# Performance work log

Hardware: AMD Instinct MI355X
Metric: run time of the kernel (lower is better)

Reference implementation:

```python
import jax, jax.numpy as jnp
import numpy as np

T, B, V, E, HID, K = 1024, 128, 65536, 128, 256, 64
H = HID // 2  # per-direction LSTM hidden


def setup_inputs() -> dict:
    key = jax.random.key(0)
    ks = jax.random.split(key, 18)
    s = 0.05
    f32 = jnp.float32
    return {
        "kmers": jax.random.randint(ks[0], (T, B), 0, V),
        "tags": jax.random.randint(ks[1], (B,), 0, K),
        "emb": jax.random.normal(ks[2], (V, E), f32) * s,
        "w_ih_f": jax.random.normal(ks[3], (4 * H, E), f32) * s,
        "w_hh_f": jax.random.normal(ks[4], (4 * H, H), f32) * s,
        "b_ih_f": jax.random.normal(ks[5], (4 * H,), f32) * s,
        "b_hh_f": jax.random.normal(ks[6], (4 * H,), f32) * s,
        "w_ih_b": jax.random.normal(ks[7], (4 * H, E), f32) * s,
        "w_hh_b": jax.random.normal(ks[8], (4 * H, H), f32) * s,
        "b_ih_b": jax.random.normal(ks[9], (4 * H,), f32) * s,
        "b_hh_b": jax.random.normal(ks[10], (4 * H,), f32) * s,
        "w_proj": jax.random.normal(ks[11], (K, HID), f32) * s,
        "b_proj": jax.random.normal(ks[12], (K,), f32) * s,
        "start_trans": jax.random.uniform(ks[13], (K,), f32, -0.1, 0.1),
        "end_trans": jax.random.uniform(ks[14], (K,), f32, -0.1, 0.1),
        "trans": jax.random.uniform(ks[15], (K, K), f32, -0.1, 0.1),
    }


def _lstm_dir(x, w_ih, w_hh, b_ih, b_hh):
    # x: [T, B, E] -> hidden states [T, B, H]; PyTorch gate order i,f,g,o
    b = b_ih + b_hh
    xg = jnp.einsum('tbe,ge->tbg', x, w_ih) + b  # precompute input gates
    Bd = x.shape[1]
    Hd = w_hh.shape[1]
    def step(carry, g_in):
        h, c = carry
        g = g_in + h @ w_hh.T
        i, f, gg, o = jnp.split(g, 4, axis=-1)
        c = jax.nn.sigmoid(f) * c + jax.nn.sigmoid(i) * jnp.tanh(gg)
        h = jax.nn.sigmoid(o) * jnp.tanh(c)
        return (h, c), h
    init = (jnp.zeros((Bd, Hd), x.dtype), jnp.zeros((Bd, Hd), x.dtype))
    _, hs = jax.lax.scan(step, init, xg)
    return hs


def reference(kmers, tags, emb, w_ih_f, w_hh_f, b_ih_f, b_hh_f,
              w_ih_b, w_hh_b, b_ih_b, b_hh_b, w_proj, b_proj,
              start_trans, end_trans, trans):
    x = emb[kmers]  # [T, B, E]
    h_f = _lstm_dir(x, w_ih_f, w_hh_f, b_ih_f, b_hh_f)
    h_b = _lstm_dir(x[::-1], w_ih_b, w_hh_b, b_ih_b, b_hh_b)[::-1]
    out = jnp.concatenate([h_f, h_b], axis=-1)  # [T, B, HID]
    emissions = jnp.einsum('tbh,kh->tbk', out, w_proj) + b_proj  # [T, B, K]

    # tags repeated along time (original: tags.repeat(sent_size, 1))
    tags_seq = jnp.broadcast_to(tags[None, :], (emissions.shape[0], tags.shape[0]))

    # CRF numerator: score of given tag sequence (full mask)
    em_sel = jnp.take_along_axis(emissions, tags_seq[:, :, None], axis=2)[..., 0]  # [T, B]
    numerator = (start_trans[tags_seq[0]] + em_sel.sum(0)
                 + trans[tags_seq[:-1], tags_seq[1:]].sum(0)
                 + end_trans[tags_seq[-1]])  # [B]

    # CRF denominator: forward algorithm (log partition)
    def fwd_step(score, em_t):
        # score: [B, K] -> logsumexp over previous tag
        nxt = jax.nn.logsumexp(score[:, :, None] + trans[None, :, :] + em_t[:, None, :], axis=1)
        return nxt, None
    init = start_trans[None, :] + emissions[0]  # [B, K]
    final, _ = jax.lax.scan(fwd_step, init, emissions[1:])
    denominator = jax.nn.logsumexp(final + end_trans[None, :], axis=1)  # [B]

    # torchcrf default reduction='sum'; module returns negated llh
    return (denominator - numerator).sum()
```

## Files before the change

kernel.cpp:

```cpp
#include <hip/hip_runtime.h>
#include <hip/hip_bf16.h>

typedef _Float16 half8_t __attribute__((ext_vector_type(8)));
typedef _Float16 half4_t __attribute__((ext_vector_type(4)));
typedef _Float16 half2_t __attribute__((ext_vector_type(2)));
typedef float float4_t __attribute__((ext_vector_type(4)));
typedef unsigned int uint2_t __attribute__((ext_vector_type(2)));

#define TT 1024
#define BB 128
#define EE 128
#define HH 128
#define NTAG 64
#define ASTR 144

__device__ __forceinline__ float fast_exp(float x) {
  return __builtin_amdgcn_exp2f(x * 1.44269504088896f);
}
__device__ __forceinline__ void lds_barrier() {
  asm volatile("s_waitcnt lgkmcnt(0)\n\ts_barrier" ::: "memory");
}
__device__ __forceinline__ half2_t cvt_pk(float a, float b) {
  return __builtin_bit_cast(half2_t, __builtin_amdgcn_cvt_pkrtz(a, b));
}
__device__ __forceinline__ half2_t h2bc(float v) {
  _Float16 h = (_Float16)v;
  half2_t r; r[0] = h; r[1] = h;
  return r;
}
__device__ __forceinline__ float quad_max4(float v) {
  unsigned a = __builtin_bit_cast(unsigned, v);
  uint2_t r = __builtin_amdgcn_permlane32_swap(a, a, false, false);
  float m = fmaxf(__builtin_bit_cast(float, r[0]), __builtin_bit_cast(float, r[1]));
  unsigned b = __builtin_bit_cast(unsigned, m);
  uint2_t s = __builtin_amdgcn_permlane16_swap(b, b, false, false);
  return fmaxf(__builtin_bit_cast(float, s[0]), __builtin_bit_cast(float, s[1]));
}
__device__ __forceinline__ half2_t tanh6(half2_t x) {
  half2_t y = __builtin_elementwise_min(__builtin_elementwise_max(x, h2bc(-1.6f)), h2bc(1.6f));
  half2_t u = y * y;
  half2_t p = u * h2bc(0.04667f) + h2bc(-0.28507f);
  p = u * p + h2bc(1.0f);
  return y * p;
}
__device__ __forceinline__ half2_t sig6(half2_t x) {
  half2_t y = __builtin_elementwise_min(__builtin_elementwise_max(x, h2bc(-3.2f)), h2bc(3.2f));
  half2_t u = y * y;
  half2_t q = u * h2bc(0.00072921875f) + h2bc(-0.017816875f);
  q = u * q + h2bc(0.25f);
  return y * q + h2bc(0.5f);
}

__global__ __launch_bounds__(256) void init_kernel(float4_t* __restrict__ p) {
  p[blockIdx.x * 256 + threadIdx.x] = (float4_t){0.f, 0.f, 0.f, 0.f};
}

__global__ __launch_bounds__(256) void embed_kernel(const int* __restrict__ kmers,
                                                    const float* __restrict__ emb,
                                                    half4_t* __restrict__ x) {
  const int g = blockIdx.x * 256 + threadIdx.x;
  const int row = g >> 5, seg = g & 31;
  const int km = kmers[row];
  const float4_t v = ((const float4_t*)(emb + (size_t)km * EE))[seg];
  half4_t o;
  o[0] = (_Float16)v[0]; o[1] = (_Float16)v[1];
  o[2] = (_Float16)v[2]; o[3] = (_Float16)v[3];
  x[(size_t)row * 32 + seg] = o;
}

__device__ __forceinline__ void xg_body(
    int wg, const _Float16* __restrict__ x,
    const float* __restrict__ w_ih_f, const float* __restrict__ b_ih_f, const float* __restrict__ b_hh_f,
    const float* __restrict__ w_ih_b, const float* __restrict__ b_ih_b, const float* __restrict__ b_hh_b,
    _Float16* __restrict__ xgbuf, int s, int Tseg) {
  const int nt = Tseg >> 4;
  const int dir = wg / (8 * nt);
  const int rem = wg - dir * 8 * nt;
  const int chunk = rem / nt;
  const int tb = rem - chunk * nt;
  const int tid = threadIdx.x;
  const int wave = tid >> 6, lane = tid & 63;
  const int n16 = lane & 15, quad = lane >> 4;

  const float* wih = dir ? w_ih_b : w_ih_f;
  const float* bih = dir ? b_ih_b : b_ih_f;
  const float* bhh = dir ? b_hh_b : b_hh_f;

  half8_t wf[4][4];
#pragma unroll
  for (int g = 0; g < 4; ++g) {
    const int row = g * HH + wave * 16 + n16;
#pragma unroll
    for (int kf = 0; kf < 4; ++kf) {
      const float* src = wih + row * EE + kf * 32 + quad * 8;
#pragma unroll
      for (int i = 0; i < 8; ++i) wf[g][kf][i] = (_Float16)src[i];
    }
  }
  float4_t bias4[4];
#pragma unroll
  for (int g = 0; g < 4; ++g) {
    const int row = g * HH + wave * 16 + quad * 4;
    const float4_t bi = *(const float4_t*)(bih + row);
    const float4_t bh = *(const float4_t*)(bhh + row);
    bias4[g] = bi + bh;
  }

  const int l0 = tb * 16;
  half8_t xb[4];
  {
    const int te = dir ? (TT - 1 - (s * Tseg + l0)) : (s * Tseg + l0);
#pragma unroll
    for (int kf = 0; kf < 4; ++kf)
      xb[kf] = *(const half8_t*)(x + ((size_t)te * BB + chunk * 16 + n16) * EE + kf * 32 + quad * 8);
  }
  for (int u = 0; u < 16; ++u) {
    const int l = l0 + u;
    half8_t xn[4] = {};
    if (u < 15) {
      const int tn = dir ? (TT - 1 - (s * Tseg + l + 1)) : (s * Tseg + l + 1);
#pragma unroll
      for (int kf = 0; kf < 4; ++kf)
        xn[kf] = *(const half8_t*)(x + ((size_t)tn * BB + chunk * 16 + n16) * EE + kf * 32 + quad * 8);
    }
    float4_t acc[4];
#pragma unroll
    for (int g = 0; g < 4; ++g) acc[g] = bias4[g];
#pragma unroll
    for (int kf = 0; kf < 4; ++kf)
#pragma unroll
      for (int g = 0; g < 4; ++g)
        acc[g] = __builtin_amdgcn_mfma_f32_16x16x32_f16(wf[g][kf], xb[kf], acc[g], 0, 0, 0);
    half8_t ho0, ho1;
#pragma unroll
    for (int r = 0; r < 4; ++r) {
      ho0[r] = (_Float16)acc[0][r];
      ho0[4 + r] = (_Float16)acc[1][r];
      ho1[r] = (_Float16)acc[2][r];
      ho1[4 + r] = (_Float16)acc[3][r];
    }
    _Float16* ob = xgbuf + (size_t)dir * Tseg * 65536 + (size_t)l * 65536 + chunk * 8192 +
                   wave * 1024 + lane * 16;
    *(half8_t*)ob = ho0;
    *(half8_t*)(ob + 8) = ho1;
#pragma unroll
    for (int kf = 0; kf < 4; ++kf) xb[kf] = xn[kf];
  }
}

__global__ __launch_bounds__(512) void xg_kernel(
    const _Float16* __restrict__ x,
    const float* __restrict__ w_ih_f, const float* __restrict__ b_ih_f, const float* __restrict__ b_hh_f,
    const float* __restrict__ w_ih_b, const float* __restrict__ b_ih_b, const float* __restrict__ b_hh_b,
    _Float16* __restrict__ xgbuf, int s, int Tseg) {
  xg_body(blockIdx.x, x, w_ih_f, b_ih_f, b_hh_f, w_ih_b, b_ih_b, b_hh_b, xgbuf, s, Tseg);
}

__global__ __launch_bounds__(512, 2) void lstm_xg_kernel(
    const _Float16* __restrict__ xgrd, _Float16* __restrict__ xgwr,
    const _Float16* __restrict__ x,
    const float* __restrict__ w_hh_f, const float* __restrict__ w_hh_b,
    const float* __restrict__ w_ih_f, const float* __restrict__ b_ih_f, const float* __restrict__ b_hh_f,
    const float* __restrict__ w_ih_b, const float* __restrict__ b_ih_b, const float* __restrict__ b_hh_b,
    _Float16* __restrict__ h_cat, _Float16* __restrict__ h_state, float* __restrict__ c_state,
    int s, int sx, int Tseg) {
  __shared__ _Float16 A[2][16 * ASTR];
  if (blockIdx.x >= 16) {
    xg_body(blockIdx.x - 16, x, w_ih_f, b_ih_f, b_hh_f, w_ih_b, b_ih_b, b_hh_b, xgwr, sx, Tseg);
    return;
  }
  const int wg = blockIdx.x;
  const int dir = wg >> 3, chunk = wg & 7;
  const int b0 = chunk * 16;
  const float* w_hh = dir ? w_hh_b : w_hh_f;
  const int tid = threadIdx.x;
  const int wave = tid >> 6, lane = tid & 63;
  const int n16 = lane & 15, quad = lane >> 4;

  half8_t wf[4][4];
#pragma unroll
  for (int g = 0; g < 4; ++g) {
    const int row = g * HH + wave * 16 + n16;
#pragma unroll
    for (int kf = 0; kf < 4; ++kf) {
      const float* src = w_hh + row * HH + kf * 32 + quad * 8;
#pragma unroll
      for (int i = 0; i < 8; ++i) wf[g][kf][i] = (_Float16)src[i];
    }
  }
  const int sidx = ((wg * 8 + wave) * 64 + lane) * 4;
  half4_t h4 = *(const half4_t*)(h_state + sidx);
  float4_t c4 = *(const float4_t*)(c_state + sidx);
  half2_t c2[2];
  c2[0] = cvt_pk(c4[0], c4[1]);
  c2[1] = cvt_pk(c4[2], c4[3]);
  *(half4_t*)(&A[0][n16 * ASTR + wave * 16 + quad * 4]) = h4;

  const _Float16* xgw =
      xgrd + (size_t)dir * Tseg * 65536 + chunk * 8192 + wave * 1024 + (size_t)lane * 16;
  half4_t hlast = h4;
  const float4_t z4 = {0.f, 0.f, 0.f, 0.f};
  const int te0 = dir ? (TT - 1 - s * Tseg) : (s * Tseg);
  _Float16* gp_run =
      h_cat + ((size_t)te0 * BB + b0 + n16) * 256 + dir * HH + wave * 16 + quad * 4;
  const ptrdiff_t dstep = dir ? -(ptrdiff_t)32768 : (ptrdiff_t)32768;

  half8_t pf0[4], pf1[4];
#pragma unroll
  for (int j = 0; j < 4; ++j) {
    const _Float16* p = xgw + (size_t)j * 65536;
    pf0[j] = *(const half8_t*)p;
    pf1[j] = *(const half8_t*)(p + 8);
  }

#define LSTM_STEP(AB, AN, X0, X1)                                                          \
  {                                                                                        \
    const _Float16* Abp = &AB[0];                                                          \
    _Float16* Anp = &AN[0];                                                                \
    half8_t hb0 = *(const half8_t*)(Abp + n16 * ASTR + 0 * 32 + quad * 8);                 \
    half8_t hb1 = *(const half8_t*)(Abp + n16 * ASTR + 1 * 32 + quad * 8);                 \
    half8_t hb2 = *(const half8_t*)(Abp + n16 * ASTR + 2 * 32 + quad * 8);                 \
    half8_t hb3 = *(const half8_t*)(Abp + n16 * ASTR + 3 * 32 + quad * 8);                 \
    float4_t acc[4];                                                                       \
    _Pragma("unroll") for (int g = 0; g < 4; ++g) {                                        \
      acc[g] = __builtin_amdgcn_mfma_f32_16x16x32_f16(wf[g][0], hb0, z4, 0, 0, 0);         \
    }                                                                                      \
    _Pragma("unroll") for (int g = 0; g < 4; ++g) {                                        \
      acc[g] = __builtin_amdgcn_mfma_f32_16x16x32_f16(wf[g][1], hb1, acc[g], 0, 0, 0);     \
    }                                                                                      \
    _Pragma("unroll") for (int g = 0; g < 4; ++g) {                                        \
      acc[g] = __builtin_amdgcn_mfma_f32_16x16x32_f16(wf[g][2], hb2, acc[g], 0, 0, 0);     \
    }                                                                                      \
    _Pragma("unroll") for (int g = 0; g < 4; ++g) {                                        \
      acc[g] = __builtin_amdgcn_mfma_f32_16x16x32_f16(wf[g][3], hb3, acc[g], 0, 0, 0);     \
    }                                                                                      \
    const half2_t* x0p = (const half2_t*)&X0;                                              \
    const half2_t* x1p = (const half2_t*)&X1;                                              \
    half4_t hstore;                                                                        \
    _Pragma("unroll") for (int p = 0; p < 2; ++p) {                                        \
      const half2_t i_ = sig6(cvt_pk(acc[0][2 * p], acc[0][2 * p + 1]) + x0p[p]);          \
      const half2_t f_ = sig6(cvt_pk(acc[1][2 * p], acc[1][2 * p + 1]) + x0p[2 + p]);      \
      const half2_t g_ = tanh6(cvt_pk(acc[2][2 * p], acc[2][2 * p + 1]) + x1p[p]);         \
      const half2_t o_ = sig6(cvt_pk(acc[3][2 * p], acc[3][2 * p + 1]) + x1p[2 + p]);      \
      c2[p] = f_ * c2[p] + i_ * g_;                                                        \
      const half2_t hh = o_ * tanh6(c2[p]);                                                \
      hstore[2 * p] = hh[0];                                                               \
      hstore[2 * p + 1] = hh[1];                                                           \
    }                                                                                      \
    *(half4_t*)(Anp + n16 * ASTR + wave * 16 + quad * 4) = hstore;                         \
    *(half4_t*)gp_run = hstore;                                                            \
    hlast = hstore;                                                                        \
  }

  for (int il = 0; il < Tseg - 4; il += 4) {
#pragma unroll
    for (int j = 0; j < 4; ++j) {
      lds_barrier();
      if (j & 1) {
        LSTM_STEP(A[1], A[0], pf0[j], pf1[j]);
      } else {
        LSTM_STEP(A[0], A[1], pf0[j], pf1[j]);
      }
      const _Float16* p = xgw + (size_t)(il + j + 4) * 65536;
      pf0[j] = *(const half8_t*)p;
      pf1[j] = *(const half8_t*)(p + 8);
      gp_run += dstep;
    }
  }
#pragma unroll
  for (int j = 0; j < 4; ++j) {
    lds_barrier();
    if (j & 1) {
      LSTM_STEP(A[1], A[0], pf0[j], pf1[j]);
    } else {
      LSTM_STEP(A[0], A[1], pf0[j], pf1[j]);
    }
    gp_run += dstep;
  }
#undef LSTM_STEP

  *(half4_t*)(h_state + sidx) = hlast;
  c4[0] = (float)c2[0][0]; c4[1] = (float)c2[0][1];
  c4[2] = (float)c2[1][0]; c4[3] = (float)c2[1][1];
  *(float4_t*)(c_state + sidx) = c4;
}

__global__ __launch_bounds__(256) void emis_kernel(const _Float16* __restrict__ h_cat,
                                                   const float* __restrict__ w_proj,
                                                   const float* __restrict__ b_proj,
                                                   float* __restrict__ em,
                                                   _Float16* __restrict__ expem) {
  const int tid = threadIdx.x;
  const int wave = tid >> 6, lane = tid & 63;
  const int n16 = lane & 15, quad = lane >> 4;
  const size_t row0 = (size_t)blockIdx.x * 64 + wave * 16;

  half8_t bf[4][8];
#pragma unroll
  for (int nt = 0; nt < 4; ++nt) {
    const float* wp = w_proj + (nt * 16 + n16) * 256;
#pragma unroll
    for (int kf = 0; kf < 8; ++kf) {
      const int kb = kf * 32 + quad * 8;
#pragma unroll
      for (int i = 0; i < 8; ++i) bf[nt][kf][i] = (_Float16)wp[kb + i];
    }
  }
  float4_t acc[4];
#pragma unroll
  for (int nt = 0; nt < 4; ++nt) {
    const float bv = b_proj[nt * 16 + n16];
    acc[nt] = (float4_t){bv, bv, bv, bv};
  }
#pragma unroll
  for (int kf = 0; kf < 8; ++kf) {
    half8_t af = *(const half8_t*)(h_cat + (row0 + n16) * 256 + kf * 32 + quad * 8);
#pragma unroll
    for (int nt = 0; nt < 4; ++nt)
      acc[nt] = __builtin_amdgcn_mfma_f32_16x16x32_f16(af, bf[nt][kf], acc[nt], 0, 0, 0);
  }
#pragma unroll
  for (int nt = 0; nt < 4; ++nt)
#pragma unroll
    for (int r = 0; r < 4; ++r) {
      const size_t idx = (row0 + quad * 4 + r) * NTAG + nt * 16 + n16;
      em[idx] = acc[nt][r];
      expem[idx] = (_Float16)fast_exp(acc[nt][r]);
    }
}

__global__ __launch_bounds__(64) void crf_kernel(const float* __restrict__ em,
                                                 const _Float16* __restrict__ expem,
                                                 const float* __restrict__ trans,
                                                 const float* __restrict__ start_trans,
                                                 const float* __restrict__ end_trans,
                                                 _Float16* __restrict__ amid,
                                                 float* __restrict__ scmid) {
  const int lane = threadIdx.x;
  const int n16 = lane & 15, quad = lane >> 4;
  const int side = blockIdx.x >> 3;
  const int bg = blockIdx.x & 7;
  const int gb = bg * 16 + n16;

  half8_t efA[4][2];
#pragma unroll
  for (int mt = 0; mt < 4; ++mt)
#pragma unroll
    for (int kf = 0; kf < 2; ++kf)
#pragma unroll
      for (int i = 0; i < 8; ++i) {
        const int m = mt * 16 + n16, k = kf * 32 + quad * 8 + i;
        const float tv = side ? trans[m * NTAG + k] : trans[k * NTAG + m];
        efA[mt][kf][i] = (_Float16)(fast_exp(tv) * 0.015625f);
      }

  float sv[16];
#pragma unroll
  for (int kf = 0; kf < 2; ++kf) {
    const int j0 = kf * 32 + quad * 8;
#pragma unroll
    for (int i = 0; i < 8; ++i)
      sv[kf * 8 + i] =
          side ? end_trans[j0 + i] : (start_trans[j0 + i] + em[(size_t)gb * NTAG + j0 + i]);
  }
  float m0;
  {
    float mx[8];
#pragma unroll
    for (int i = 0; i < 8; ++i) mx[i] = fmaxf(sv[i], sv[8 + i]);
#pragma unroll
    for (int i = 0; i < 4; ++i) mx[i] = fmaxf(mx[i], mx[4 + i]);
    m0 = fmaxf(fmaxf(mx[0], mx[1]), fmaxf(mx[2], mx[3]));
    m0 = quad_max4(m0);
  }
  half8_t pb[2];
#pragma unroll
  for (int kf = 0; kf < 2; ++kf)
#pragma unroll
    for (int i = 0; i < 8; ++i) pb[kf][i] = (_Float16)fast_exp(sv[kf * 8 + i] - m0);
  float lz2 = 0.f;
  const float4_t z4 = {0.f, 0.f, 0.f, 0.f};
  const _Float16* exb = expem + (size_t)gb * NTAG;

#define CRF_CORE(PB0, PB1)                                                                 \
    float4_t a0 = __builtin_amdgcn_mfma_f32_16x16x32_f16(efA[0][0], PB0, z4, 0, 0, 0);     \
    float4_t a1 = __builtin_amdgcn_mfma_f32_16x16x32_f16(efA[1][0], PB0, z4, 0, 0, 0);     \
    float4_t a2 = __builtin_amdgcn_mfma_f32_16x16x32_f16(efA[2][0], PB0, z4, 0, 0, 0);     \
    float4_t a3 = __builtin_amdgcn_mfma_f32_16x16x32_f16(efA[3][0], PB0, z4, 0, 0, 0);     \
    a0 = __builtin_amdgcn_mfma_f32_16x16x32_f16(efA[0][1], PB1, a0, 0, 0, 0);              \
    a1 = __builtin_amdgcn_mfma_f32_16x16x32_f16(efA[1][1], PB1, a1, 0, 0, 0);              \
    a2 = __builtin_amdgcn_mfma_f32_16x16x32_f16(efA[2][1], PB1, a2, 0, 0, 0);              \
    a3 = __builtin_amdgcn_mfma_f32_16x16x32_f16(efA[3][1], PB1, a3, 0, 0, 0);              \
    half2_t dpk[4][2];                                                                     \
    dpk[0][0] = cvt_pk(a0[0], a0[1]); dpk[0][1] = cvt_pk(a0[2], a0[3]);                    \
    dpk[1][0] = cvt_pk(a1[0], a1[1]); dpk[1][1] = cvt_pk(a1[2], a1[3]);                    \
    dpk[2][0] = cvt_pk(a2[0], a2[1]); dpk[2][1] = cvt_pk(a2[2], a2[3]);                    \
    dpk[3][0] = cvt_pk(a3[0], a3[1]); dpk[3][1] = cvt_pk(a3[2], a3[3]);                    \
    half2_t ww[2][4];                                                                      \
    _Pragma("unroll") for (int kf = 0; kf < 2; ++kf)                                       \
      _Pragma("unroll") for (int p = 0; p < 2; ++p) {                                      \
        const unsigned Xu = __builtin_bit_cast(unsigned, dpk[2 * kf][p]);                  \
        const unsigned Yu = __builtin_bit_cast(unsigned, dpk[2 * kf + 1][p]);              \
        uint2_t r1 = __builtin_amdgcn_permlane32_swap(Xu, Yu, false, false);               \
        uint2_t r2 = __builtin_amdgcn_permlane16_swap(r1[0], r1[1], false, false);         \
        ww[kf][p] = __builtin_bit_cast(half2_t, r2[0]);                                    \
        ww[kf][2 + p] = __builtin_bit_cast(half2_t, r2[1]);                                \
      }

#define CRF_RESCALE(TCUR)                                                                  \
    if (((TCUR) & 15) == 0) {                                                              \
      half2_t* pw0 = (half2_t*)&pb[0];                                                     \
      half2_t* pw1 = (half2_t*)&pb[1];                                                     \
      half2_t m2 = __builtin_elementwise_max(pw0[0], pw0[1]);                              \
      m2 = __builtin_elementwise_max(m2, __builtin_elementwise_max(pw0[2], pw0[3]));       \
      m2 = __builtin_elementwise_max(m2, __builtin_elementwise_max(pw1[0], pw1[1]));       \
      m2 = __builtin_elementwise_max(m2, __builtin_elementwise_max(pw1[2], pw1[3]));       \
      float mm = fmaxf((float)m2[0], (float)m2[1]);                                        \
      mm = quad_max4(mm);                                                                  \
      lz2 += __builtin_amdgcn_logf(mm);                                                    \
      const half2_t rc = h2bc(__builtin_amdgcn_rcpf(mm));                                  \
      _Pragma("unroll") for (int j2 = 0; j2 < 4; ++j2) { pw0[j2] *= rc; pw1[j2] *= rc; }   \
    }

#define FWD_STEP(TCUR, GC0, GC1)                                                           \
  {                                                                                        \
    CRF_CORE(pb[0], pb[1])                                                                 \
    const half2_t* gw0 = (const half2_t*)&GC0;                                             \
    const half2_t* gw1 = (const half2_t*)&GC1;                                             \
    half2_t* pw0 = (half2_t*)&pb[0];                                                       \
    half2_t* pw1 = (half2_t*)&pb[1];                                                       \
    _Pragma("unroll") for (int w2 = 0; w2 < 4; ++w2) {                                     \
      pw0[w2] = ww[0][w2] * gw0[w2];                                                       \
      pw1[w2] = ww[1][w2] * gw1[w2];                                                       \
    }                                                                                      \
    CRF_RESCALE(TCUR)                                                                      \
  }

#define BWD_STEP(TCUR, GC0, GC1)                                                           \
  {                                                                                        \
    const half8_t pg0 = pb[0] * GC0;                                                       \
    const half8_t pg1 = pb[1] * GC1;                                                       \
    CRF_CORE(pg0, pg1)                                                                     \
    half2_t* pw0 = (half2_t*)&pb[0];                                                       \
    half2_t* pw1 = (half2_t*)&pb[1];                                                       \
    _Pragma("unroll") for (int w2 = 0; w2 < 4; ++w2) {                                     \
      pw0[w2] = ww[0][w2];                                                                 \
      pw1[w2] = ww[1][w2];                                                                 \
    }                                                                                      \
    CRF_RESCALE(TCUR)                                                                      \
  }

  half8_t pre0[8], pre1[8];
  if (side == 0) {
#pragma unroll
    for (int j = 0; j < 8; ++j) {
      pre0[j] = *(const half8_t*)(exb + (size_t)(1 + j) * 8192 + quad * 8);
      pre1[j] = *(const half8_t*)(exb + (size_t)(1 + j) * 8192 + 32 + quad * 8);
    }
    int t = 1;
    for (int grp = 0; grp < 64; ++grp) {
#pragma unroll
      for (int j = 0; j < 8; ++j) {
        const half8_t gc0 = pre0[j], gc1 = pre1[j];
        int tf = t + 8; tf = tf > 1023 ? 1023 : tf;
        pre0[j] = *(const half8_t*)(exb + (size_t)tf * 8192 + quad * 8);
        pre1[j] = *(const half8_t*)(exb + (size_t)tf * 8192 + 32 + quad * 8);
        FWD_STEP(t, gc0, gc1)
        ++t;
      }
    }
  } else {
#pragma unroll
    for (int j = 0; j < 8; ++j) {
      pre0[j] = *(const half8_t*)(exb + (size_t)(1023 - j) * 8192 + quad * 8);
      pre1[j] = *(const half8_t*)(exb + (size_t)(1023 - j) * 8192 + 32 + quad * 8);
    }
    int t = 1023;
    for (int grp = 0; grp < 63; ++grp) {
#pragma unroll
      for (int j = 0; j < 8; ++j) {
        const half8_t gc0 = pre0[j], gc1 = pre1[j];
        int tf = t - 8; tf = tf < 0 ? 0 : tf;
        pre0[j] = *(const half8_t*)(exb + (size_t)tf * 8192 + quad * 8);
        pre1[j] = *(const half8_t*)(exb + (size_t)tf * 8192 + 32 + quad * 8);
        BWD_STEP(t, gc0, gc1)
        --t;
      }
    }
    for (; t >= 513; --t) {
      const half8_t gc0 = *(const half8_t*)(exb + (size_t)t * 8192 + quad * 8);
      const half8_t gc1 = *(const half8_t*)(exb + (size_t)t * 8192 + 32 + quad * 8);
      BWD_STEP(t, gc0, gc1)
    }
  }
#undef FWD_STEP
#undef BWD_STEP
#undef CRF_RESCALE
#undef CRF_CORE

  _Float16* ap = amid + (size_t)(side * BB + gb) * NTAG;
  *(half8_t*)(ap + quad * 8) = pb[0];
  *(half8_t*)(ap + 32 + quad * 8) = pb[1];
  if (quad == 0)
    scmid[side * BB + gb] = m0 + 0.693147180559945f * lz2;
}

__global__ __launch_bounds__(256) void numer_kernel(const float* __restrict__ em,
                                                    const int* __restrict__ tags,
                                                    const float* __restrict__ trans,
                                                    const float* __restrict__ start_trans,
                                                    const float* __restrict__ end_trans,
                                                    float* __restrict__ num) {
  const int b = blockIdx.x;
  const int tg = tags[b];
  float acc = 0.f;
  for (int t = threadIdx.x; t < TT; t += 256)
    acc += em[((size_t)t * BB + b) * NTAG + tg];
#pragma unroll
  for (int off = 32; off > 0; off >>= 1) acc += __shfl_xor(acc, off, 64);
  __shared__ float red[4];
  if ((threadIdx.x & 63) == 0) red[threadIdx.x >> 6] = acc;
  __syncthreads();
  if (threadIdx.x == 0) {
    const float tot = red[0] + red[1] + red[2] + red[3];
    num[b] = start_trans[tg] + end_trans[tg] + 1023.0f * trans[tg * NTAG + tg] + tot;
  }
}

__global__ __launch_bounds__(128) void final_kernel(const _Float16* __restrict__ amid,
                                                    const float* __restrict__ scmid,
                                                    const float* __restrict__ num,
                                                    float* __restrict__ out) {
  const int b = threadIdx.x;
  const _Float16* af = amid + (size_t)b * NTAG;
  const _Float16* bf = amid + (size_t)(BB + b) * NTAG;
  float dot = 0.f;
#pragma unroll
  for (int kf = 0; kf < 8; ++kf) {
    const half8_t av = *(const half8_t*)(af + kf * 8);
    const half8_t bv = *(const half8_t*)(bf + kf * 8);
#pragma unroll
    for (int i = 0; i < 8; ++i) dot += (float)av[i] * (float)bv[i];
  }
  const float denomv = scmid[b] + scmid[BB + b] +
                       0.693147180559945f * (6138.0f + __builtin_amdgcn_logf(dot));
  float v = denomv - num[b];
#pragma unroll
  for (int off = 32; off > 0; off >>= 1) v += __shfl_xor(v, off, 64);
  __shared__ float red[2];
  if ((b & 63) == 0) red[b >> 6] = v;
  __syncthreads();
  if (b == 0) out[0] = red[0] + red[1];
}

extern "C" void kernel_launch(void* const* d_in, const int* in_sizes, int n_in,
                              void* d_out, int out_size, void* d_ws, size_t ws_size,
                              hipStream_t stream) {
  const int* kmers = (const int*)d_in[0];
  const int* tags = (const int*)d_in[1];
  const float* emb = (const float*)d_in[2];
  const float* w_ih_f = (const float*)d_in[3];
  const float* w_hh_f = (const float*)d_in[4];
  const float* b_ih_f = (const float*)d_in[5];
  const float* b_hh_f = (const float*)d_in[6];
  const float* w_ih_b = (const float*)d_in[7];
  const float* w_hh_b = (const float*)d_in[8];
  const float* b_ih_b = (const float*)d_in[9];
  const float* b_hh_b = (const float*)d_in[10];
  const float* w_proj = (const float*)d_in[11];
  const float* b_proj = (const float*)d_in[12];
  const float* start_trans = (const float*)d_in[13];
  const float* end_trans = (const float*)d_in[14];
  const float* trans = (const float*)d_in[15];

  char* ws = (char*)d_ws;
  half4_t* x = (half4_t*)ws;
  _Float16* h_cat = (_Float16*)(ws + 33554432);
  float* em = (float*)ws;
  float* out = (float*)d_out;

  const bool fused = ws_size >= 235078656ull;
  if (fused) {
    const int Tseg = 256;
    _Float16* buf0 = (_Float16*)(ws + 100663296);
    _Float16* buf1 = (_Float16*)(ws + 100663296 + 67108864);
    _Float16* expem = (_Float16*)(ws + 100663296);
    _Float16* h_state = (_Float16*)(ws + 100663296 + 134217728);
    float* c_state = (float*)(ws + 100663296 + 134217728 + 65536);
    _Float16* amid = (_Float16*)(ws + 100663296 + 134217728);
    float* scmid = (float*)(ws + 100663296 + 134217728 + 32768);
    float* num = (float*)(ws + 100663296 + 134217728 + 196608);

    hipLaunchKernelGGL(init_kernel, dim3(48), dim3(256), 0, stream, (float4_t*)h_state);
    hipLaunchKernelGGL(embed_kernel, dim3(16384), dim3(256), 0, stream, kmers, emb, x);
    hipLaunchKernelGGL(xg_kernel, dim3(Tseg), dim3(512), 0, stream, (const _Float16*)x,
                       w_ih_f, b_ih_f, b_hh_f, w_ih_b, b_ih_b, b_hh_b, buf0, 0, Tseg);
    for (int s = 0; s < 3; ++s) {
      _Float16* rd = (s & 1) ? buf1 : buf0;
      _Float16* wr = (s & 1) ? buf0 : buf1;
      hipLaunchKernelGGL(lstm_xg_kernel, dim3(16 + Tseg), dim3(512), 0, stream,
                         (const _Float16*)rd, wr, (const _Float16*)x, w_hh_f, w_hh_b,
                         w_ih_f, b_ih_f, b_hh_f, w_ih_b, b_ih_b, b_hh_b,
                         h_cat, h_state, c_state, s, s + 1, Tseg);
    }
    hipLaunchKernelGGL(lstm_xg_kernel, dim3(16), dim3(512), 0, stream,
                       (const _Float16*)buf1, buf0, (const _Float16*)x, w_hh_f, w_hh_b,
                       w_ih_f, b_ih_f, b_hh_f, w_ih_b, b_ih_b, b_hh_b,
                       h_cat, h_state, c_state, 3, 0, Tseg);
    hipLaunchKernelGGL(emis_kernel, dim3(2048), dim3(256), 0, stream, h_cat, w_proj, b_proj, em,
                       expem);
    hipLaunchKernelGGL(crf_kernel, dim3(16), dim3(64), 0, stream, em, (const _Float16*)expem,
                       trans, start_trans, end_trans, amid, scmid);
    hipLaunchKernelGGL(numer_kernel, dim3(128), dim3(256), 0, stream, em, tags, trans,
                       start_trans, end_trans, num);
    hipLaunchKernelGGL(final_kernel, dim3(1), dim3(128), 0, stream, amid, scmid, num, out);
  } else {
    int nseg;
    if (ws_size >= 167969792ull) nseg = 4;
    else if (ws_size >= 134415360ull) nseg = 8;
    else nseg = 16;
    const int Tseg = TT / nseg;
    const size_t xg_bytes = 268435456ull / (size_t)nseg;
    _Float16* xgbuf = (_Float16*)(ws + 100663296);
    _Float16* expem = (_Float16*)(ws + 100663296);
    _Float16* h_state = (_Float16*)(ws + 100663296 + xg_bytes);
    float* c_state = (float*)(ws + 100663296 + xg_bytes + 65536);
    _Float16* amid = (_Float16*)(ws + 100663296 + xg_bytes);
    float* scmid = (float*)(ws + 100663296 + xg_bytes + 32768);
    float* num = (float*)(ws + 100663296 + xg_bytes + 196608);

    hipLaunchKernelGGL(init_kernel, dim3(48), dim3(256), 0, stream, (float4_t*)h_state);
    hipLaunchKernelGGL(embed_kernel, dim3(16384), dim3(256), 0, stream, kmers, emb, x);
    for (int s = 0; s < nseg; ++s) {
      hipLaunchKernelGGL(xg_kernel, dim3(Tseg), dim3(512), 0, stream, (const _Float16*)x,
                         w_ih_f, b_ih_f, b_hh_f, w_ih_b, b_ih_b, b_hh_b, xgbuf, s, Tseg);
      hipLaunchKernelGGL(lstm_xg_kernel, dim3(16), dim3(512), 0, stream,
                         (const _Float16*)xgbuf, xgbuf, (const _Float16*)x, w_hh_f, w_hh_b,
                         w_ih_f, b_ih_f, b_hh_f, w_ih_b, b_ih_b, b_hh_b,
                         h_cat, h_state, c_state, s, s, Tseg);
    }
    hipLaunchKernelGGL(emis_kernel, dim3(2048), dim3(256), 0, stream, h_cat, w_proj, b_proj, em,
                       expem);
    hipLaunchKernelGGL(crf_kernel, dim3(16), dim3(64), 0, stream, em, (const _Float16*)expem,
                       trans, start_trans, end_trans, amid, scmid);
    hipLaunchKernelGGL(numer_kernel, dim3(128), dim3(256), 0, stream, em, tags, trans,
                       start_trans, end_trans, num);
    hipLaunchKernelGGL(final_kernel, dim3(1), dim3(128), 0, stream, amid, scmid, num, out);
  }
}
```

Before: 954.2 us.

## Parallelize CRF forward recursion via segmented transfer-matrix products and merge

Replaces the 16-block sequential CRF forward/backward scan with 2048 blocks, each computing the 64x64 product of scaled transition-times-emission matrices over a 64-step time segment per batch element, starting from the identity. A new merge kernel chains the 16 segment matrices per batch element with a vector, tracking log scales. The numerator computation is folded into extra blocks of the same launch. The intent is to cut the serial CRF latency tail, which used only 16 wavefronts. In exchange each block does four times the MFMA work of a vector recursion, and fp16 matrix products with periodic rescaling risk precision loss.

```diff
diff --git a/kernel.cpp b/kernel.cpp
--- a/kernel.cpp
+++ b/kernel.cpp
@@ -20,12 +20,22 @@
 __device__ __forceinline__ void lds_barrier() {
   asm volatile("s_waitcnt lgkmcnt(0)\n\ts_barrier" ::: "memory");
 }
+__device__ __forceinline__ void lds_fence() {
+  asm volatile("s_waitcnt lgkmcnt(0)" ::: "memory");
+}
 __device__ __forceinline__ half2_t cvt_pk(float a, float b) {
   return __builtin_bit_cast(half2_t, __builtin_amdgcn_cvt_pkrtz(a, b));
 }
 __device__ __forceinline__ half2_t h2bc(float v) {
   _Float16 h = (_Float16)v;
   half2_t r; r[0] = h; r[1] = h;
+  return r;
+}
+__device__ __forceinline__ half8_t h8bc(float v) {
+  _Float16 h = (_Float16)v;
+  half8_t r;
+#pragma unroll
+  for (int i = 0; i < 8; ++i) r[i] = h;
   return r;
 }
 __device__ __forceinline__ float quad_max4(float v) {
@@ -329,18 +339,31 @@
     }
 }
 
-__global__ __launch_bounds__(64) void crf_kernel(const float* __restrict__ em,
-                                                 const _Float16* __restrict__ expem,
-                                                 const float* __restrict__ trans,
-                                                 const float* __restrict__ start_trans,
-                                                 const float* __restrict__ end_trans,
-                                                 _Float16* __restrict__ amid,
-                                                 float* __restrict__ scmid) {
+__global__ __launch_bounds__(64) void mcrf_kernel(const float* __restrict__ em,
+                                                  const _Float16* __restrict__ expem,
+                                                  const float* __restrict__ trans,
+                                                  const int* __restrict__ tags,
+                                                  const float* __restrict__ start_trans,
+                                                  const float* __restrict__ end_trans,
+                                                  _Float16* __restrict__ Nbuf,
+                                                  float* __restrict__ lzbuf,
+                                                  float* __restrict__ num) {
   const int lane = threadIdx.x;
+  if (blockIdx.x >= 2048) {
+    const int nb = blockIdx.x - 2048;
+    const int tg = tags[nb];
+    float acc = 0.f;
+    for (int t = lane; t < TT; t += 64)
+      acc += em[((size_t)t * BB + nb) * NTAG + tg];
+#pragma unroll
+    for (int off = 32; off > 0; off >>= 1) acc += __shfl_xor(acc, off, 64);
+    if (lane == 0)
+      num[nb] = start_trans[tg] + end_trans[tg] + 1023.0f * trans[tg * NTAG + tg] + acc;
+    return;
+  }
   const int n16 = lane & 15, quad = lane >> 4;
-  const int side = blockIdx.x >> 3;
-  const int bg = blockIdx.x & 7;
-  const int gb = bg * 16 + n16;
+  const int b = blockIdx.x >> 4;
+  const int s = blockIdx.x & 15;
 
   half8_t efA[4][2];
 #pragma unroll
@@ -350,39 +373,28 @@
 #pragma unroll
       for (int i = 0; i < 8; ++i) {
         const int m = mt * 16 + n16, k = kf * 32 + quad * 8 + i;
-        const float tv = side ? trans[m * NTAG + k] : trans[k * NTAG + m];
-        efA[mt][kf][i] = (_Float16)(fast_exp(tv) * 0.015625f);
+        efA[mt][kf][i] = (_Float16)(fast_exp(trans[k * NTAG + m]) * 0.015625f);
       }
 
-  float sv[16];
-#pragma unroll
-  for (int kf = 0; kf < 2; ++kf) {
-    const int j0 = kf * 32 + quad * 8;
-#pragma unroll
-    for (int i = 0; i < 8; ++i)
-      sv[kf * 8 + i] =
-          side ? end_trans[j0 + i] : (start_trans[j0 + i] + em[(size_t)gb * NTAG + j0 + i]);
-  }
-  float m0;
-  {
-    float mx[8];
-#pragma unroll
-    for (int i = 0; i < 8; ++i) mx[i] = fmaxf(sv[i], sv[8 + i]);
-#pragma unroll
-    for (int i = 0; i < 4; ++i) mx[i] = fmaxf(mx[i], mx[4 + i]);
-    m0 = fmaxf(fmaxf(mx[0], mx[1]), fmaxf(mx[2], mx[3]));
-    m0 = quad_max4(m0);
-  }
-  half8_t pb[2];
-#pragma unroll
-  for (int kf = 0; kf < 2; ++kf)
-#pragma unroll
-    for (int i = 0; i < 8; ++i) pb[kf][i] = (_Float16)fast_exp(sv[kf * 8 + i] - m0);
+  half8_t pb[4][2];
+#pragma unroll
+  for (int tile = 0; tile < 4; ++tile)
+#pragma unroll
+    for (int kf = 0; kf < 2; ++kf)
+#pragma unroll
+      for (int i = 0; i < 8; ++i) {
+        const int k = kf * 32 + quad * 8 + i;
+        pb[tile][kf][i] = (_Float16)((k == tile * 16 + n16) ? 1.f : 0.f);
+      }
+
   float lz2 = 0.f;
   const float4_t z4 = {0.f, 0.f, 0.f, 0.f};
-  const _Float16* exb = expem + (size_t)gb * NTAG;
-
-#define CRF_CORE(PB0, PB1)                                                                 \
+  const _Float16* exb = expem + (size_t)b * NTAG;
+  const int t0 = s * 64 + 1;
+  const int nsteps = (s == 15) ? 63 : 64;
+
+#define MCRF_CORE(PB0, PB1, NB0, NB1)                                                      \
+  {                                                                                        \
     float4_t a0 = __builtin_amdgcn_mfma_f32_16x16x32_f16(efA[0][0], PB0, z4, 0, 0, 0);     \
     float4_t a1 = __builtin_amdgcn_mfma_f32_16x16x32_f16(efA[1][0], PB0, z4, 0, 0, 0);     \
     float4_t a2 = __builtin_amdgcn_mfma_f32_16x16x32_f16(efA[2][0], PB0, z4, 0, 0, 0);     \
@@ -396,161 +408,143 @@
     dpk[1][0] = cvt_pk(a1[0], a1[1]); dpk[1][1] = cvt_pk(a1[2], a1[3]);                    \
     dpk[2][0] = cvt_pk(a2[0], a2[1]); dpk[2][1] = cvt_pk(a2[2], a2[3]);                    \
     dpk[3][0] = cvt_pk(a3[0], a3[1]); dpk[3][1] = cvt_pk(a3[2], a3[3]);                    \
-    half2_t ww[2][4];                                                                      \
-    _Pragma("unroll") for (int kf = 0; kf < 2; ++kf)                                       \
+    half2_t* wwp0 = (half2_t*)&NB0;                                                        \
+    half2_t* wwp1 = (half2_t*)&NB1;                                                        \
+    _Pragma("unroll") for (int kf = 0; kf < 2; ++kf) {                                     \
+      half2_t* wp = kf ? wwp1 : wwp0;                                                      \
       _Pragma("unroll") for (int p = 0; p < 2; ++p) {                                      \
         const unsigned Xu = __builtin_bit_cast(unsigned, dpk[2 * kf][p]);                  \
         const unsigned Yu = __builtin_bit_cast(unsigned, dpk[2 * kf + 1][p]);              \
         uint2_t r1 = __builtin_amdgcn_permlane32_swap(Xu, Yu, false, false);               \
         uint2_t r2 = __builtin_amdgcn_permlane16_swap(r1[0], r1[1], false, false);         \
-        ww[kf][p] = __builtin_bit_cast(half2_t, r2[0]);                                    \
-        ww[kf][2 + p] = __builtin_bit_cast(half2_t, r2[1]);                                \
-      }
-
-#define CRF_RESCALE(TCUR)                                                                  \
-    if (((TCUR) & 15) == 0) {                                                              \
-      half2_t* pw0 = (half2_t*)&pb[0];                                                     \
-      half2_t* pw1 = (half2_t*)&pb[1];                                                     \
-      half2_t m2 = __builtin_elementwise_max(pw0[0], pw0[1]);                              \
-      m2 = __builtin_elementwise_max(m2, __builtin_elementwise_max(pw0[2], pw0[3]));       \
-      m2 = __builtin_elementwise_max(m2, __builtin_elementwise_max(pw1[0], pw1[1]));       \
-      m2 = __builtin_elementwise_max(m2, __builtin_elementwise_max(pw1[2], pw1[3]));       \
-      float mm = fmaxf((float)m2[0], (float)m2[1]);                                        \
+        wp[p] = __builtin_bit_cast(half2_t, r2[0]);                                        \
+        wp[2 + p] = __builtin_bit_cast(half2_t, r2[1]);                                    \
+      }                                                                                    \
+    }                                                                                      \
+  }
+
+#define MSTEP(GC0, GC1, IT)                                                                \
+  {                                                                                        \
+    _Pragma("unroll") for (int tile = 0; tile < 4; ++tile) {                               \
+      half8_t nb0, nb1;                                                                    \
+      MCRF_CORE(pb[tile][0], pb[tile][1], nb0, nb1)                                        \
+      pb[tile][0] = nb0 * GC0;                                                             \
+      pb[tile][1] = nb1 * GC1;                                                             \
+    }                                                                                      \
+    if (((IT) & 15) == 15) {                                                               \
+      half8_t m8 = __builtin_elementwise_max(pb[0][0], pb[0][1]);                          \
+      m8 = __builtin_elementwise_max(m8, __builtin_elementwise_max(pb[1][0], pb[1][1]));   \
+      m8 = __builtin_elementwise_max(m8, __builtin_elementwise_max(pb[2][0], pb[2][1]));   \
+      m8 = __builtin_elementwise_max(m8, __builtin_elementwise_max(pb[3][0], pb[3][1]));   \
+      float mm = (float)m8[0];                                                             \
+      _Pragma("unroll") for (int i = 1; i < 8; ++i) mm = fmaxf(mm, (float)m8[i]);          \
       mm = quad_max4(mm);                                                                  \
+      mm = fmaxf(mm, __shfl_xor(mm, 1, 64));                                               \
+      mm = fmaxf(mm, __shfl_xor(mm, 2, 64));                                               \
+      mm = fmaxf(mm, __shfl_xor(mm, 4, 64));                                               \
+      mm = fmaxf(mm, __shfl_xor(mm, 8, 64));                                               \
       lz2 += __builtin_amdgcn_logf(mm);                                                    \
-      const half2_t rc = h2bc(__builtin_amdgcn_rcpf(mm));                                  \
-      _Pragma("unroll") for (int j2 = 0; j2 < 4; ++j2) { pw0[j2] *= rc; pw1[j2] *= rc; }   \
-    }
-
-#define FWD_STEP(TCUR, GC0, GC1)                                                           \
-  {                                                                                        \
-    CRF_CORE(pb[0], pb[1])                                                                 \
-    const half2_t* gw0 = (const half2_t*)&GC0;                                             \
-    const half2_t* gw1 = (const half2_t*)&GC1;                                             \
-    half2_t* pw0 = (half2_t*)&pb[0];                                                       \
-    half2_t* pw1 = (half2_t*)&pb[1];                                                       \
-    _Pragma("unroll") for (int w2 = 0; w2 < 4; ++w2) {                                     \
-      pw0[w2] = ww[0][w2] * gw0[w2];                                                       \
-      pw1[w2] = ww[1][w2] * gw1[w2];                                                       \
-    }                                                                                      \
-    CRF_RESCALE(TCUR)                                                                      \
-  }
-
-#define BWD_STEP(TCUR, GC0, GC1)                                                           \
-  {                                                                                        \
-    const half8_t pg0 = pb[0] * GC0;                                                       \
-    const half8_t pg1 = pb[1] * GC1;                                                       \
-    CRF_CORE(pg0, pg1)                                                                     \
-    half2_t* pw0 = (half2_t*)&pb[0];                                                       \
-    half2_t* pw1 = (half2_t*)&pb[1];                                                       \
-    _Pragma("unroll") for (int w2 = 0; w2 < 4; ++w2) {                                     \
-      pw0[w2] = ww[0][w2];                                                                 \
-      pw1[w2] = ww[1][w2];                                                                 \
-    }                                                                                      \
-    CRF_RESCALE(TCUR)                                                                      \
-  }
-
-  half8_t pre0[8], pre1[8];
-  if (side == 0) {
-#pragma unroll
-    for (int j = 0; j < 8; ++j) {
-      pre0[j] = *(const half8_t*)(exb + (size_t)(1 + j) * 8192 + quad * 8);
-      pre1[j] = *(const half8_t*)(exb + (size_t)(1 + j) * 8192 + 32 + quad * 8);
-    }
-    int t = 1;
-    for (int grp = 0; grp < 64; ++grp) {
-#pragma unroll
-      for (int j = 0; j < 8; ++j) {
-        const half8_t gc0 = pre0[j], gc1 = pre1[j];
-        int tf = t + 8; tf = tf > 1023 ? 1023 : tf;
-        pre0[j] = *(const half8_t*)(exb + (size_t)tf * 8192 + quad * 8);
-        pre1[j] = *(const half8_t*)(exb + (size_t)tf * 8192 + 32 + quad * 8);
-        FWD_STEP(t, gc0, gc1)
-        ++t;
-      }
-    }
-  } else {
-#pragma unroll
-    for (int j = 0; j < 8; ++j) {
-      pre0[j] = *(const half8_t*)(exb + (size_t)(1023 - j) * 8192 + quad * 8);
-      pre1[j] = *(const half8_t*)(exb + (size_t)(1023 - j) * 8192 + 32 + quad * 8);
-    }
-    int t = 1023;
-    for (int grp = 0; grp < 63; ++grp) {
-#pragma unroll
-      for (int j = 0; j < 8; ++j) {
-        const half8_t gc0 = pre0[j], gc1 = pre1[j];
-        int tf = t - 8; tf = tf < 0 ? 0 : tf;
-        pre0[j] = *(const half8_t*)(exb + (size_t)tf * 8192 + quad * 8);
-        pre1[j] = *(const half8_t*)(exb + (size_t)tf * 8192 + 32 + quad * 8);
-        BWD_STEP(t, gc0, gc1)
-        --t;
-      }
-    }
-    for (; t >= 513; --t) {
-      const half8_t gc0 = *(const half8_t*)(exb + (size_t)t * 8192 + quad * 8);
-      const half8_t gc1 = *(const half8_t*)(exb + (size_t)t * 8192 + 32 + quad * 8);
-      BWD_STEP(t, gc0, gc1)
-    }
-  }
-#undef FWD_STEP
-#undef BWD_STEP
-#undef CRF_RESCALE
-#undef CRF_CORE
-
-  _Float16* ap = amid + (size_t)(side * BB + gb) * NTAG;
-  *(half8_t*)(ap + quad * 8) = pb[0];
-  *(half8_t*)(ap + 32 + quad * 8) = pb[1];
-  if (quad == 0)
-    scmid[side * BB + gb] = m0 + 0.693147180559945f * lz2;
-}
-
-__global__ __launch_bounds__(256) void numer_kernel(const float* __restrict__ em,
-                                                    const int* __restrict__ tags,
-                                                    const float* __restrict__ trans,
-                                                    const float* __restrict__ start_trans,
-                                                    const float* __restrict__ end_trans,
-                                                    float* __restrict__ num) {
-  const int b = blockIdx.x;
-  const int tg = tags[b];
-  float acc = 0.f;
-  for (int t = threadIdx.x; t < TT; t += 256)
-    acc += em[((size_t)t * BB + b) * NTAG + tg];
-#pragma unroll
-  for (int off = 32; off > 0; off >>= 1) acc += __shfl_xor(acc, off, 64);
-  __shared__ float red[4];
-  if ((threadIdx.x & 63) == 0) red[threadIdx.x >> 6] = acc;
-  __syncthreads();
-  if (threadIdx.x == 0) {
-    const float tot = red[0] + red[1] + red[2] + red[3];
-    num[b] = start_trans[tg] + end_trans[tg] + 1023.0f * trans[tg * NTAG + tg] + tot;
-  }
-}
-
-__global__ __launch_bounds__(128) void final_kernel(const _Float16* __restrict__ amid,
-                                                    const float* __restrict__ scmid,
+      const half8_t rc8 = h8bc(__builtin_amdgcn_rcpf(mm));                                 \
+      _Pragma("unroll") for (int tile = 0; tile < 4; ++tile) {                             \
+        pb[tile][0] *= rc8;                                                                \
+        pb[tile][1] *= rc8;                                                                \
+      }                                                                                    \
+    }                                                                                      \
+  }
+
+  half8_t pre0[4], pre1[4];
+#pragma unroll
+  for (int j = 0; j < 4; ++j) {
+    const size_t tt = (size_t)(t0 + j) * 8192;
+    pre0[j] = *(const half8_t*)(exb + tt + quad * 8);
+    pre1[j] = *(const half8_t*)(exb + tt + 32 + quad * 8);
+  }
+  int it = 0;
+  const int full4 = nsteps >> 2;
+  for (int grp = 0; grp < full4; ++grp) {
+#pragma unroll
+    for (int j = 0; j < 4; ++j) {
+      const half8_t gc0 = pre0[j], gc1 = pre1[j];
+      int tf = t0 + it + 4;
+      tf = tf > 1023 ? 1023 : tf;
+      const size_t tt = (size_t)tf * 8192;
+      pre0[j] = *(const half8_t*)(exb + tt + quad * 8);
+      pre1[j] = *(const half8_t*)(exb + tt + 32 + quad * 8);
+      MSTEP(gc0, gc1, it)
+      ++it;
+    }
+  }
+  for (; it < nsteps; ++it) {
+    const size_t tt = (size_t)(t0 + it) * 8192;
+    const half8_t gc0 = *(const half8_t*)(exb + tt + quad * 8);
+    const half8_t gc1 = *(const half8_t*)(exb + tt + 32 + quad * 8);
+    MSTEP(gc0, gc1, it)
+  }
+#undef MSTEP
+#undef MCRF_CORE
+
+  _Float16* nb = Nbuf + ((size_t)b * 16 + s) * 4096;
+#pragma unroll
+  for (int tile = 0; tile < 4; ++tile) {
+    const int col = tile * 16 + n16;
+#pragma unroll
+    for (int kf = 0; kf < 2; ++kf)
+      *(half8_t*)(nb + (size_t)col * 64 + kf * 32 + quad * 8) = pb[tile][kf];
+  }
+  if (lane == 0) lzbuf[b * 16 + s] = lz2;
+}
+
+__global__ __launch_bounds__(64) void merge_kernel(const _Float16* __restrict__ Nbuf,
+                                                   const float* __restrict__ lzbuf,
+                                                   const float* __restrict__ em,
+                                                   const float* __restrict__ start_trans,
+                                                   const float* __restrict__ end_trans,
+                                                   float* __restrict__ denom) {
+  const int b = blockIdx.x, m = threadIdx.x;
+  __shared__ float w[64];
+  float L2 = 0.f;
+  w[m] = fast_exp(end_trans[m]);
+  for (int s = 15; s >= 0; --s) {
+    lds_fence();
+    const _Float16* row = Nbuf + (((size_t)b * 16 + s) * 64 + m) * 64;
+    float acc = 0.f;
+#pragma unroll
+    for (int kf = 0; kf < 8; ++kf) {
+      const half8_t rv = *(const half8_t*)(row + kf * 8);
+#pragma unroll
+      for (int i = 0; i < 8; ++i) acc += (float)rv[i] * w[kf * 8 + i];
+    }
+    float mx = acc;
+#pragma unroll
+    for (int off = 32; off > 0; off >>= 1) mx = fmaxf(mx, __shfl_xor(mx, off, 64));
+    L2 += __builtin_amdgcn_logf(mx) + lzbuf[b * 16 + s];
+    const float inv = __builtin_amdgcn_rcpf(mx);
+    lds_fence();
+    w[m] = acc * inv;
+  }
+  lds_fence();
+  const float sv = start_trans[m] + em[(size_t)b * NTAG + m];
+  float m0 = sv;
+#pragma unroll
+  for (int off = 32; off > 0; off >>= 1) m0 = fmaxf(m0, __shfl_xor(m0, off, 64));
+  float z = fast_exp(sv - m0) * w[m];
+#pragma unroll
+  for (int off = 32; off > 0; off >>= 1) z += __shfl_xor(z, off, 64);
+  if (m == 0)
+    denom[b] = m0 + 0.693147180559945f * (L2 + 6138.0f + __builtin_amdgcn_logf(z));
+}
+
+__global__ __launch_bounds__(128) void final_kernel(const float* __restrict__ denom,
                                                     const float* __restrict__ num,
                                                     float* __restrict__ out) {
-  const int b = threadIdx.x;
-  const _Float16* af = amid + (size_t)b * NTAG;
-  const _Float16* bf = amid + (size_t)(BB + b) * NTAG;
-  float dot = 0.f;
-#pragma unroll
-  for (int kf = 0; kf < 8; ++kf) {
-    const half8_t av = *(const half8_t*)(af + kf * 8);
-    const half8_t bv = *(const half8_t*)(bf + kf * 8);
-#pragma unroll
-    for (int i = 0; i < 8; ++i) dot += (float)av[i] * (float)bv[i];
-  }
-  const float denomv = scmid[b] + scmid[BB + b] +
-                       0.693147180559945f * (6138.0f + __builtin_amdgcn_logf(dot));
-  float v = denomv - num[b];
+  const int tid = threadIdx.x;
+  float v = denom[tid] - num[tid];
 #pragma unroll
   for (int off = 32; off > 0; off >>= 1) v += __shfl_xor(v, off, 64);
   __shared__ float red[2];
-  if ((b & 63) == 0) red[b >> 6] = v;
+  if ((tid & 63) == 0) red[tid >> 6] = v;
   __syncthreads();
-  if (b == 0) out[0] = red[0] + red[1];
+  if (tid == 0) out[0] = red[0] + red[1];
 }
 
 extern "C" void kernel_launch(void* const* d_in, const int* in_sizes, int n_in,
@@ -578,6 +572,10 @@
   _Float16* h_cat = (_Float16*)(ws + 33554432);
   float* em = (float*)ws;
   float* out = (float*)d_out;
+  _Float16* Nbuf = (_Float16*)(ws + 33554432);
+  float* lzbuf = (float*)(ws + 33554432 + 16777216);
+  float* denom = (float*)(ws + 33554432 + 16785408);
+  float* num = (float*)(ws + 33554432 + 16785920);
 
   const bool fused = ws_size >= 235078656ull;
   if (fused) {
@@ -587,9 +585,6 @@
     _Float16* expem = (_Float16*)(ws + 100663296);
     _Float16* h_state = (_Float16*)(ws + 100663296 + 134217728);
     float* c_state = (float*)(ws + 100663296 + 134217728 + 65536);
-    _Float16* amid = (_Float16*)(ws + 100663296 + 134217728);
-    float* scmid = (float*)(ws + 100663296 + 134217728 + 32768);
-    float* num = (float*)(ws + 100663296 + 134217728 + 196608);
 
     hipLaunchKernelGGL(init_kernel, dim3(48), dim3(256), 0, stream, (float4_t*)h_state);
     hipLaunchKernelGGL(embed_kernel, dim3(16384), dim3(256), 0, stream, kmers, emb, x);
@@ -609,11 +604,12 @@
                        h_cat, h_state, c_state, 3, 0, Tseg);
     hipLaunchKernelGGL(emis_kernel, dim3(2048), dim3(256), 0, stream, h_cat, w_proj, b_proj, em,
                        expem);
-    hipLaunchKernelGGL(crf_kernel, dim3(16), dim3(64), 0, stream, em, (const _Float16*)expem,
-                       trans, start_trans, end_trans, amid, scmid);
-    hipLaunchKernelGGL(numer_kernel, dim3(128), dim3(256), 0, stream, em, tags, trans,
-                       start_trans, end_trans, num);
-    hipLaunchKernelGGL(final_kernel, dim3(1), dim3(128), 0, stream, amid, scmid, num, out);
+    hipLaunchKernelGGL(mcrf_kernel, dim3(2176), dim3(64), 0, stream, em,
+                       (const _Float16*)expem, trans, tags, start_trans, end_trans, Nbuf, lzbuf,
+                       num);
+    hipLaunchKernelGGL(merge_kernel, dim3(128), dim3(64), 0, stream, (const _Float16*)Nbuf,
+                       lzbuf, em, start_trans, end_trans, denom);
+    hipLaunchKernelGGL(final_kernel, dim3(1), dim3(128), 0, stream, denom, num, out);
   } else {
     int nseg;
     if (ws_size >= 167969792ull) nseg = 4;
@@ -625,9 +621,6 @@
     _Float16* expem = (_Float16*)(ws + 100663296);
     _Float16* h_state = (_Float16*)(ws + 100663296 + xg_bytes);
     float* c_state = (float*)(ws + 100663296 + xg_bytes + 65536);
-    _Float16* amid = (_Float16*)(ws + 100663296 + xg_bytes);
-    float* scmid = (float*)(ws + 100663296 + xg_bytes + 32768);
-    float* num = (float*)(ws + 100663296 + xg_bytes + 196608);
 
     hipLaunchKernelGGL(init_kernel, dim3(48), dim3(256), 0, stream, (float4_t*)h_state);
     hipLaunchKernelGGL(embed_kernel, dim3(16384), dim3(256), 0, stream, kmers, emb, x);
@@ -641,10 +634,11 @@
     }
     hipLaunchKernelGGL(emis_kernel, dim3(2048), dim3(256), 0, stream, h_cat, w_proj, b_proj, em,
                        expem);
-    hipLaunchKernelGGL(crf_kernel, dim3(16), dim3(64), 0, stream, em, (const _Float16*)expem,
-                       trans, start_trans, end_trans, amid, scmid);
-    hipLaunchKernelGGL(numer_kernel, dim3(128), dim3(256), 0, stream, em, tags, trans,
-                       start_trans, end_trans, num);
-    hipLaunchKernelGGL(final_kernel, dim3(1), dim3(128), 0, stream, amid, scmid, num, out);
-  }
-}
+    hipLaunchKernelGGL(mcrf_kernel, dim3(2176), dim3(64), 0, stream, em,
+                       (const _Float16*)expem, trans, tags, start_trans, end_trans, Nbuf, lzbuf,
+                       num);
+    hipLaunchKernelGGL(merge_kernel, dim3(128), dim3(64), 0, stream, (const _Float16*)Nbuf,
+                       lzbuf, em, start_trans, end_trans, denom);
+    hipLaunchKernelGGL(final_kernel, dim3(1), dim3(128), 0, stream, denom, num, out);
+  }
+}
```

Measured after the change: 959.7 us. No clear change (+0.6%).
